# Optimization experiments

Hardware: AMD Instinct MI355X
Metric: run time of the kernel (lower is better)

## Reference

```python
import jax, jax.numpy as jnp
from jax import lax
import numpy as np

B, S, H = 8, 512, 768


def setup_inputs() -> dict:
    key = jax.random.key(0)
    ks = jax.random.split(key, 8)
    outputs = jax.random.normal(ks[0], (B, S, H), dtype=jnp.float32)
    starts = jax.random.randint(ks[1], (B,), S // 4, 3 * S // 4)
    mask = jnp.stack([starts, jnp.full((B,), S, dtype=starts.dtype)], axis=1)  # [B,2]
    sc = 1.0 / np.sqrt(H)
    Wa_w = jax.random.normal(ks[2], (H, H), dtype=jnp.float32) * sc
    Wa_b = jax.random.normal(ks[3], (H,), dtype=jnp.float32) * sc
    Ua_w = jax.random.normal(ks[4], (H, H), dtype=jnp.float32) * sc
    Ua_b = jax.random.normal(ks[5], (H,), dtype=jnp.float32) * sc
    Va_w = jax.random.normal(ks[6], (1, H), dtype=jnp.float32) * sc
    Va_b = jax.random.normal(ks[7], (1,), dtype=jnp.float32) * sc
    return {"outputs": outputs, "mask": mask, "Wa_w": Wa_w, "Wa_b": Wa_b,
            "Ua_w": Ua_w, "Ua_b": Ua_b, "Va_w": Va_w, "Va_b": Va_b}


def reference(outputs, mask, Wa_w, Wa_b, Ua_w, Ua_b, Va_w, Va_b):
    # outputs: [B,S,H]; mask[:,0] = start (source = tokens [0:start], summary = [start:S])
    b, s, h = outputs.shape
    Wq = jnp.einsum('bsh,oh->bso', outputs, Wa_w) + Wa_b  # query proj, [B,S,H]
    Uk = jnp.einsum('bsh,oh->bso', outputs, Ua_w) + Ua_b  # key proj,   [B,S,H]
    va = Va_w[0]  # [H]
    vb = Va_b[0]

    # Stream over query token positions to avoid a [B,S,S,H] tanh intermediate.
    def step(_, wq_t):  # wq_t: [B,H]
        m = jnp.tanh(wq_t[:, None, :] + Uk)          # [B,S,H]
        sc_t = jnp.einsum('bkh,h->bk', m, va) + vb   # [B,S]
        return None, sc_t

    _, scores = lax.scan(step, None, jnp.swapaxes(Wq, 0, 1))  # [S(query token), B, S(key)]
    scores = jnp.swapaxes(scores, 0, 1)  # [B, S_token, S_key]

    start = mask[:, 0]                              # [B]
    j = jnp.arange(s)
    # summary query j corresponds to token index start + j
    t_idx = jnp.clip(start[:, None] + j[None, :], 0, s - 1)            # [B,S]
    sc = jnp.take_along_axis(scores, t_idx[:, :, None], axis=1)       # [B,S,S]
    key_mask = (j[None, :] < start[:, None])                           # [B,S] valid source keys
    q_mask = (j[None, :] < (s - start)[:, None])                       # [B,S] valid summary queries

    sc = jnp.where(key_mask[:, None, :], sc, -1e30)
    w = jax.nn.softmax(sc, axis=-1)
    # zero out exactly where the torch code leaves zeros
    attentions = w * key_mask[:, None, :].astype(w.dtype) * q_mask[:, :, None].astype(w.dtype)
    contexts = jnp.einsum('bjk,bkh->bjh', attentions, outputs)
    return attentions, contexts
```

## Files before the change

kernel.cpp:

```cpp
#include <hip/hip_runtime.h>

typedef float  f32x4   __attribute__((ext_vector_type(4)));
typedef short  short8  __attribute__((ext_vector_type(8)));
typedef unsigned short ushort8 __attribute__((ext_vector_type(8)));

constexpr int kB = 8;
constexpr int kS = 512;
constexpr int kH = 768;

constexpr float kTanhScale = 2.8853900817779268f;

__device__ __forceinline__ float native_exp2(float x) {
    float r; asm("v_exp_f32 %0, %1" : "=v"(r) : "v"(x)); return r;
}

__device__ __forceinline__ float waveMax(float v) {
#pragma unroll
    for (int off = 32; off > 0; off >>= 1) v = fmaxf(v, __shfl_xor(v, off, 64));
    return v;
}
__device__ __forceinline__ float waveSum(float v) {
#pragma unroll
    for (int off = 32; off > 0; off >>= 1) v += __shfl_xor(v, off, 64);
    return v;
}

__device__ __forceinline__ void cvt16(const float4* v, unsigned short* hb, unsigned short* lb) {
#pragma unroll
    for (int q = 0; q < 4; ++q) {
#pragma unroll
        for (int c = 0; c < 4; ++c) {
            float x = (&v[q].x)[c];
            unsigned u = __float_as_uint(x);
            hb[q * 4 + c] = (unsigned short)(u >> 16);
            float hf = __uint_as_float(u & 0xFFFF0000u);
            lb[q * 4 + c] = (unsigned short)(__float_as_uint(x - hf) >> 16);
        }
    }
}

__global__ __launch_bounds__(256) void k1_mfma(
    const float* __restrict__ A,
    const float* __restrict__ W0, const float* __restrict__ b0,
    const float* __restrict__ W1, const float* __restrict__ b1,
    float* __restrict__ eq, float* __restrict__ ekT)
{
    __shared__ char smem[49664];
    unsigned short* Ahi = (unsigned short*)smem;
    unsigned short* Alo = (unsigned short*)(smem + 10240);
    unsigned short* Bhi = (unsigned short*)(smem + 20480);
    unsigned short* Blo = (unsigned short*)(smem + 28160);

    const int z = blockIdx.z;
    const float* W    = z ? W1 : W0;
    const float* bias = z ? b1 : b0;

    const int m0 = blockIdx.y * 128;
    const int n0 = blockIdx.x * 96;
    const int t  = threadIdx.x;

    const int ar = t >> 1, ko = (t & 1) << 4;
    const float* agp = A + (size_t)(m0 + ar) * kH + ko;
    const float* wgp = W + (size_t)(n0 + ar) * kH + ko;
    const bool doB = (ar < 96);

    const int wid = t >> 6, lane = t & 63;
    const int wr = wid >> 1, wc = wid & 1;
    const int lr = lane & 15, lk = (lane >> 4) << 3;

    f32x4 acc[4][3];
#pragma unroll
    for (int mi = 0; mi < 4; ++mi)
#pragma unroll
        for (int ni = 0; ni < 3; ++ni)
#pragma unroll
            for (int r = 0; r < 4; ++r) acc[mi][ni][r] = 0.0f;

    for (int h0 = 0; h0 < kH; h0 += 32) {
        float4 av[4], wv[4];
#pragma unroll
        for (int q = 0; q < 4; ++q) av[q] = *(const float4*)(agp + h0 + 4 * q);
        if (doB) {
#pragma unroll
            for (int q = 0; q < 4; ++q) wv[q] = *(const float4*)(wgp + h0 + 4 * q);
        }
        __syncthreads();
        {
            unsigned short hb[16], lb[16];
            cvt16(av, hb, lb);
            *(ushort8*)(Ahi + ar * 40 + ko)     = *(ushort8*)(hb);
            *(ushort8*)(Ahi + ar * 40 + ko + 8) = *(ushort8*)(hb + 8);
            *(ushort8*)(Alo + ar * 40 + ko)     = *(ushort8*)(lb);
            *(ushort8*)(Alo + ar * 40 + ko + 8) = *(ushort8*)(lb + 8);
            if (doB) {
                cvt16(wv, hb, lb);
                *(ushort8*)(Bhi + ar * 40 + ko)     = *(ushort8*)(hb);
                *(ushort8*)(Bhi + ar * 40 + ko + 8) = *(ushort8*)(hb + 8);
                *(ushort8*)(Blo + ar * 40 + ko)     = *(ushort8*)(lb);
                *(ushort8*)(Blo + ar * 40 + ko + 8) = *(ushort8*)(lb + 8);
            }
        }
        __syncthreads();

        short8 ah[4], al_[4], bh[3], bl[3];
#pragma unroll
        for (int mi = 0; mi < 4; ++mi) {
            const int row = wr * 64 + mi * 16 + lr;
            ah[mi]  = *(const short8*)(Ahi + row * 40 + lk);
            al_[mi] = *(const short8*)(Alo + row * 40 + lk);
        }
#pragma unroll
        for (int ni = 0; ni < 3; ++ni) {
            const int row = wc * 48 + ni * 16 + lr;
            bh[ni] = *(const short8*)(Bhi + row * 40 + lk);
            bl[ni] = *(const short8*)(Blo + row * 40 + lk);
        }
#pragma unroll
        for (int mi = 0; mi < 4; ++mi)
#pragma unroll
            for (int ni = 0; ni < 3; ++ni)
                acc[mi][ni] = __builtin_amdgcn_mfma_f32_16x16x32_bf16(ah[mi], bh[ni], acc[mi][ni], 0, 0, 0);
#pragma unroll
        for (int mi = 0; mi < 4; ++mi)
#pragma unroll
            for (int ni = 0; ni < 3; ++ni)
                acc[mi][ni] = __builtin_amdgcn_mfma_f32_16x16x32_bf16(al_[mi], bh[ni], acc[mi][ni], 0, 0, 0);
#pragma unroll
        for (int mi = 0; mi < 4; ++mi)
#pragma unroll
            for (int ni = 0; ni < 3; ++ni)
                acc[mi][ni] = __builtin_amdgcn_mfma_f32_16x16x32_bf16(ah[mi], bl[ni], acc[mi][ni], 0, 0, 0);
    }

    if (z == 0) {
#pragma unroll
        for (int mi = 0; mi < 4; ++mi)
#pragma unroll
            for (int ni = 0; ni < 3; ++ni) {
                const int mg = m0 + wr * 64 + mi * 16 + ((lane >> 4) << 2);
                const int ng = n0 + wc * 48 + ni * 16 + lr;
                const float bn = bias[ng];
#pragma unroll
                for (int r = 0; r < 4; ++r)
                    eq[(size_t)(mg + r) * kH + ng] = native_exp2((acc[mi][ni][r] + bn) * kTanhScale);
            }
    } else {
        __syncthreads();
        float* stg = (float*)smem;
#pragma unroll
        for (int mi = 0; mi < 4; ++mi)
#pragma unroll
            for (int ni = 0; ni < 3; ++ni) {
                const int ml = wr * 64 + mi * 16 + ((lane >> 4) << 2);
                const int nl = wc * 48 + ni * 16 + lr;
                const float bn = bias[n0 + nl];
#pragma unroll
                for (int r = 0; r < 4; ++r)
                    stg[(ml + r) * 97 + nl] = native_exp2((acc[mi][ni][r] + bn) * kTanhScale);
            }
        __syncthreads();
        const int bI = m0 >> 9, sb = m0 & (kS - 1);
        const int s4 = (t & 31) << 2, hb_ = t >> 5;
#pragma unroll
        for (int u = 0; u < 12; ++u) {
            const int h = (u << 3) + hb_;
            float4 o = { stg[(s4 + 0) * 97 + h], stg[(s4 + 1) * 97 + h],
                         stg[(s4 + 2) * 97 + h], stg[(s4 + 3) * 97 + h] };
            *(float4*)(ekT + ((size_t)bI * kH + n0 + h) * kS + sb + s4) = o;
        }
    }
}

__global__ void k2a_worklist(const int* __restrict__ mask, int* __restrict__ wl)
{
    __shared__ int ne[kB], off[kB];
    const int tid = threadIdx.x;
    if (tid < kB) {
        int start = mask[2 * tid];
        ne[tid] = ((kS - start + 1) >> 1) * ((start + 63) >> 6);
    }
    __syncthreads();
    if (tid == 0) {
        int s = 0;
        for (int b = 0; b < kB; ++b) { off[b] = s; s += ne[b]; }
        wl[0] = s;
    }
    __syncthreads();
    for (int b = 0; b < kB; ++b) {
        int start = mask[2 * b];
        int nkw = (start + 63) >> 6;
        int n = ne[b], base = off[b];
        for (int t = tid; t < n; t += blockDim.x) {
            int jt = t / nkw, kt = t - jt * nkw;
            wl[1 + base + t] = (b << 16) | (jt << 8) | kt;
        }
    }
}

__global__ __launch_bounds__(256) void k2_scores(
    const float* __restrict__ Eq, const float* __restrict__ EkT,
    const float* __restrict__ va, const int* __restrict__ mask,
    const int* __restrict__ wl, float* __restrict__ scores)
{
    const int ntiles = wl[0];
    const int lane = threadIdx.x & 63;
    const int wslot = (blockIdx.x << 2) | (threadIdx.x >> 6);
    const int nslots = gridDim.x << 2;

    for (int w = wslot; w < ntiles; w += nslots) {
        const int e = __builtin_amdgcn_readfirstlane(wl[1 + w]);
        const int b = e >> 16, jt = (e >> 8) & 255, kt = e & 255;
        const int start = __builtin_amdgcn_readfirstlane(mask[2 * b]);
        const int jmax = kS - start;
        const int j0 = jt << 1, k0 = kt << 6;

        const float* ekp = EkT + (size_t)b * kH * kS + k0 + lane;
        int t0 = start + j0;     if (t0 > kS - 1) t0 = kS - 1;
        int t1 = start + j0 + 1; if (t1 > kS - 1) t1 = kS - 1;
        const float* eq0 = Eq + ((size_t)b * kS + t0) * kH;
        const float* eq1 = Eq + ((size_t)b * kS + t1) * kH;

        float a0 = 0.0f, a1 = 0.0f;
        float eA[8], eB[8];
#pragma unroll
        for (int c = 0; c < 8; ++c) eA[c] = ekp[(size_t)c * kS];
#pragma unroll
        for (int c = 0; c < 8; ++c) eB[c] = ekp[(size_t)(8 + c) * kS];

        for (int h0 = 0; h0 < kH; h0 += 16) {
            const bool more = (h0 + 16) < kH;
            float nA[8], nB[8];
            if (more) {
#pragma unroll
                for (int c = 0; c < 8; ++c) nA[c] = ekp[(size_t)(h0 + 16 + c) * kS];
            }
#pragma unroll
            for (int c = 0; c < 8; ++c) {
                const float vc = va[h0 + c];
                float r0 = __builtin_amdgcn_rcpf(fmaf(eq0[h0 + c], eA[c], 1.0f));
                float r1 = __builtin_amdgcn_rcpf(fmaf(eq1[h0 + c], eA[c], 1.0f));
                a0 = fmaf(vc, r0, a0);
                a1 = fmaf(vc, r1, a1);
            }
            if (more) {
#pragma unroll
                for (int c = 0; c < 8; ++c) nB[c] = ekp[(size_t)(h0 + 24 + c) * kS];
#pragma unroll
                for (int c = 0; c < 8; ++c) {
                    const float vc = va[h0 + 8 + c];
                    float r0 = __builtin_amdgcn_rcpf(fmaf(eq0[h0 + 8 + c], eB[c], 1.0f));
                    float r1 = __builtin_amdgcn_rcpf(fmaf(eq1[h0 + 8 + c], eB[c], 1.0f));
                    a0 = fmaf(vc, r0, a0);
                    a1 = fmaf(vc, r1, a1);
                }
#pragma unroll
                for (int c = 0; c < 8; ++c) { eA[c] = nA[c]; eB[c] = nB[c]; }
            } else {
#pragma unroll
                for (int c = 0; c < 8; ++c) {
                    const float vc = va[h0 + 8 + c];
                    float r0 = __builtin_amdgcn_rcpf(fmaf(eq0[h0 + 8 + c], eB[c], 1.0f));
                    float r1 = __builtin_amdgcn_rcpf(fmaf(eq1[h0 + 8 + c], eB[c], 1.0f));
                    a0 = fmaf(vc, r0, a0);
                    a1 = fmaf(vc, r1, a1);
                }
            }
        }

        float* srow = scores + ((size_t)b * kS + j0) * kS + k0 + lane;
        if (j0 < jmax)     srow[0]  = -2.0f * a0;
        if (j0 + 1 < jmax) srow[kS] = -2.0f * a1;
    }
}

__global__ __launch_bounds__(256) void k3_softmax(
    float* __restrict__ attn, const int* __restrict__ mask)
{
    const int bx = blockIdx.x;
    const int b = bx >> 9;
    const int j = bx & (kS - 1);
    const int start = mask[2 * b];
    float* row = attn + ((size_t)b * kS + j) * kS;
    const int tid = threadIdx.x;

    if (j >= kS - start) {
        row[tid] = 0.0f;
        row[tid + 256] = 0.0f;
        return;
    }

    float v0 = (tid < start) ? row[tid] : -1e30f;
    float v1 = (tid + 256 < start) ? row[tid + 256] : -1e30f;

    __shared__ float red[4];
    const int wid = tid >> 6;

    float m = waveMax(fmaxf(v0, v1));
    if ((tid & 63) == 0) red[wid] = m;
    __syncthreads();
    m = fmaxf(fmaxf(red[0], red[1]), fmaxf(red[2], red[3]));
    __syncthreads();

    float e0 = (tid < start) ? __expf(v0 - m) : 0.0f;
    float e1 = (tid + 256 < start) ? __expf(v1 - m) : 0.0f;
    float s = waveSum(e0 + e1);
    if ((tid & 63) == 0) red[wid] = s;
    __syncthreads();
    s = red[0] + red[1] + red[2] + red[3];

    float inv = __builtin_amdgcn_rcpf(s);
    row[tid] = e0 * inv;
    row[tid + 256] = e1 * inv;
}

__global__ __launch_bounds__(256) void k4_context(
    const float* __restrict__ attn, const float* __restrict__ outs,
    const int* __restrict__ mask, float* __restrict__ ctx)
{
    const int b = blockIdx.z;
    const int start = mask[2 * b];
    const int kmax = (start + 15) & ~15;
    const int m0 = blockIdx.y * 64;
    const int n0 = blockIdx.x * 64;

    __shared__ float As[16][68];
    __shared__ float Bs[16][68];

    const int tid = threadIdx.x;
    const int lrow = tid >> 2;
    const int lk4  = (tid & 3) << 2;
    const int brow = tid >> 4;
    const int bh4  = (tid & 15) << 2;
    const int is = tid >> 4;
    const int js = tid & 15;

    const float* arow = attn + ((size_t)b * kS + m0 + lrow) * kS + lk4;
    const float* bbase = outs + (size_t)b * kS * kH + n0 + bh4;

    float acc[4][4] = {};

    for (int k0 = 0; k0 < kmax; k0 += 16) {
        float4 av = *(const float4*)(arow + k0);
        float4 bv = *(const float4*)(bbase + (size_t)(k0 + brow) * kH);
        __syncthreads();
        As[lk4 + 0][lrow] = av.x;
        As[lk4 + 1][lrow] = av.y;
        As[lk4 + 2][lrow] = av.z;
        As[lk4 + 3][lrow] = av.w;
        *(float4*)&Bs[brow][bh4] = bv;
        __syncthreads();
#pragma unroll
        for (int kk = 0; kk < 16; ++kk) {
            const float* ap = &As[kk][is << 2];
            const float* bp = &Bs[kk][js << 2];
            float aa[4], bb[4];
#pragma unroll
            for (int c = 0; c < 4; ++c) { aa[c] = ap[c]; bb[c] = bp[c]; }
#pragma unroll
            for (int i = 0; i < 4; ++i)
#pragma unroll
                for (int j = 0; j < 4; ++j)
                    acc[i][j] = fmaf(aa[i], bb[j], acc[i][j]);
        }
    }

#pragma unroll
    for (int i = 0; i < 4; ++i) {
        int row = m0 + (is << 2) + i;
        float4 o = {acc[i][0], acc[i][1], acc[i][2], acc[i][3]};
        *(float4*)(ctx + ((size_t)b * kS + row) * kH + n0 + (js << 2)) = o;
    }
}

extern "C" void kernel_launch(void* const* d_in, const int* in_sizes, int n_in,
                              void* d_out, int out_size, void* d_ws, size_t ws_size,
                              hipStream_t stream)
{
    const float* outputs = (const float*)d_in[0];
    const int*   mask    = (const int*)d_in[1];
    const float* Wa_w    = (const float*)d_in[2];
    const float* Wa_b    = (const float*)d_in[3];
    const float* Ua_w    = (const float*)d_in[4];
    const float* Ua_b    = (const float*)d_in[5];
    const float* Va_w    = (const float*)d_in[6];

    float* attn = (float*)d_out;
    float* ctx  = attn + (size_t)kB * kS * kS;
    float* EkT  = ctx;

    constexpr size_t kWlBytes = 64 * 1024;
    int* wl = (int*)d_ws;
    float* Eq = (float*)((char*)d_ws + kWlBytes);

    k1_mfma<<<dim3(kH / 96, (kB * kS) / 128, 2), 256, 0, stream>>>(
        outputs, Wa_w, Wa_b, Ua_w, Ua_b, Eq, EkT);

    k2a_worklist<<<dim3(1), 256, 0, stream>>>(mask, wl);
    k2_scores<<<dim3(1024), 256, 0, stream>>>(Eq, EkT, Va_w, mask, wl, attn);

    k3_softmax<<<dim3(kB * kS), 256, 0, stream>>>(attn, mask);

    k4_context<<<dim3(kH / 64, kS / 64, kB), 256, 0, stream>>>(attn, outputs, mask, ctx);
}
```

Baseline: 161.0 us.

## Pre-split inputs to bf16 hi/lo, skip unneeded projection tiles, split scores over H

A new pre-pass kernel converts the activations and both weight matrices once into bf16 hi/lo pairs, so the GEMM no longer repeats that split per tile. The projection GEMM now exits early for row tiles that only cover masked query or key positions, and it writes compacted Eq/EkT buffers indexed by summary and source position. The score kernel splits the hidden dimension into two halves, which doubles the number of work items, writes two partial score buffers, and has the softmax add them. The cost is an extra launch, extra traffic for the converted copies and partial buffers, and scratch space borrowed from the output buffers.

```diff
diff --git a/kernel.cpp b/kernel.cpp
--- a/kernel.cpp
+++ b/kernel.cpp
@@ -7,6 +7,7 @@
 constexpr int kB = 8;
 constexpr int kS = 512;
 constexpr int kH = 768;
+constexpr int kJM = 384;
 
 constexpr float kTanhScale = 2.8853900817779268f;
 
@@ -25,25 +26,39 @@
     return v;
 }
 
-__device__ __forceinline__ void cvt16(const float4* v, unsigned short* hb, unsigned short* lb) {
-#pragma unroll
-    for (int q = 0; q < 4; ++q) {
-#pragma unroll
-        for (int c = 0; c < 4; ++c) {
-            float x = (&v[q].x)[c];
-            unsigned u = __float_as_uint(x);
-            hb[q * 4 + c] = (unsigned short)(u >> 16);
-            float hf = __uint_as_float(u & 0xFFFF0000u);
-            lb[q * 4 + c] = (unsigned short)(__float_as_uint(x - hf) >> 16);
-        }
-    }
+__global__ __launch_bounds__(256) void k0_convert(
+    const float* __restrict__ X, const float* __restrict__ Wa, const float* __restrict__ Ua,
+    unsigned short* __restrict__ Xhi, unsigned short* __restrict__ Xlo,
+    unsigned short* __restrict__ Wahi, unsigned short* __restrict__ Walo,
+    unsigned short* __restrict__ Uahi, unsigned short* __restrict__ Ualo)
+{
+    const int i4 = blockIdx.x * 256 + threadIdx.x;
+    const float* src; unsigned short *hi, *lo; int off;
+    if (i4 < 786432)      { src = X;  hi = Xhi;  lo = Xlo;  off = i4; }
+    else if (i4 < 933888) { src = Wa; hi = Wahi; lo = Walo; off = i4 - 786432; }
+    else                  { src = Ua; hi = Uahi; lo = Ualo; off = i4 - 933888; }
+
+    float4 v = *(const float4*)(src + (size_t)off * 4);
+    unsigned short h[4], l[4];
+#pragma unroll
+    for (int c = 0; c < 4; ++c) {
+        float x = (&v.x)[c];
+        unsigned u = __float_as_uint(x);
+        h[c] = (unsigned short)(u >> 16);
+        float hf = __uint_as_float(u & 0xFFFF0000u);
+        l[c] = (unsigned short)(__float_as_uint(x - hf) >> 16);
+    }
+    *(ushort4*)(hi + (size_t)off * 4) = make_ushort4(h[0], h[1], h[2], h[3]);
+    *(ushort4*)(lo + (size_t)off * 4) = make_ushort4(l[0], l[1], l[2], l[3]);
 }
 
 __global__ __launch_bounds__(256) void k1_mfma(
-    const float* __restrict__ A,
-    const float* __restrict__ W0, const float* __restrict__ b0,
-    const float* __restrict__ W1, const float* __restrict__ b1,
-    float* __restrict__ eq, float* __restrict__ ekT)
+    const unsigned short* __restrict__ Xhi, const unsigned short* __restrict__ Xlo,
+    const unsigned short* __restrict__ W0hi, const unsigned short* __restrict__ W0lo,
+    const unsigned short* __restrict__ W1hi, const unsigned short* __restrict__ W1lo,
+    const float* __restrict__ b0, const float* __restrict__ b1,
+    const int* __restrict__ mask,
+    float* __restrict__ Eqc, float* __restrict__ EkTc)
 {
     __shared__ char smem[49664];
     unsigned short* Ahi = (unsigned short*)smem;
@@ -52,17 +67,24 @@
     unsigned short* Blo = (unsigned short*)(smem + 28160);
 
     const int z = blockIdx.z;
-    const float* W    = z ? W1 : W0;
+    const unsigned short* Whi = z ? W1hi : W0hi;
+    const unsigned short* Wlo = z ? W1lo : W0lo;
     const float* bias = z ? b1 : b0;
 
     const int m0 = blockIdx.y * 128;
     const int n0 = blockIdx.x * 96;
     const int t  = threadIdx.x;
+    const int bI = m0 >> 9;
+    const int lb = m0 & (kS - 1);
+    const int start = mask[2 * bI];
+
+    if (z == 0) { if (lb + 128 <= start) return; }
+    else        { if (lb >= start) return; }
 
     const int ar = t >> 1, ko = (t & 1) << 4;
-    const float* agp = A + (size_t)(m0 + ar) * kH + ko;
-    const float* wgp = W + (size_t)(n0 + ar) * kH + ko;
     const bool doB = (ar < 96);
+    const size_t aoff = (size_t)(m0 + ar) * kH + ko;
+    const size_t woff = (size_t)(n0 + ar) * kH + ko;
 
     const int wid = t >> 6, lane = t & 63;
     const int wr = wid >> 1, wc = wid & 1;
@@ -77,28 +99,27 @@
             for (int r = 0; r < 4; ++r) acc[mi][ni][r] = 0.0f;
 
     for (int h0 = 0; h0 < kH; h0 += 32) {
-        float4 av[4], wv[4];
-#pragma unroll
-        for (int q = 0; q < 4; ++q) av[q] = *(const float4*)(agp + h0 + 4 * q);
+        ushort8 ah0 = *(const ushort8*)(Xhi + aoff + h0);
+        ushort8 ah1 = *(const ushort8*)(Xhi + aoff + h0 + 8);
+        ushort8 al0 = *(const ushort8*)(Xlo + aoff + h0);
+        ushort8 al1 = *(const ushort8*)(Xlo + aoff + h0 + 8);
+        ushort8 bh0, bh1, bl0, bl1;
         if (doB) {
-#pragma unroll
-            for (int q = 0; q < 4; ++q) wv[q] = *(const float4*)(wgp + h0 + 4 * q);
-        }
-        __syncthreads();
-        {
-            unsigned short hb[16], lb[16];
-            cvt16(av, hb, lb);
-            *(ushort8*)(Ahi + ar * 40 + ko)     = *(ushort8*)(hb);
-            *(ushort8*)(Ahi + ar * 40 + ko + 8) = *(ushort8*)(hb + 8);
-            *(ushort8*)(Alo + ar * 40 + ko)     = *(ushort8*)(lb);
-            *(ushort8*)(Alo + ar * 40 + ko + 8) = *(ushort8*)(lb + 8);
-            if (doB) {
-                cvt16(wv, hb, lb);
-                *(ushort8*)(Bhi + ar * 40 + ko)     = *(ushort8*)(hb);
-                *(ushort8*)(Bhi + ar * 40 + ko + 8) = *(ushort8*)(hb + 8);
-                *(ushort8*)(Blo + ar * 40 + ko)     = *(ushort8*)(lb);
-                *(ushort8*)(Blo + ar * 40 + ko + 8) = *(ushort8*)(lb + 8);
-            }
+            bh0 = *(const ushort8*)(Whi + woff + h0);
+            bh1 = *(const ushort8*)(Whi + woff + h0 + 8);
+            bl0 = *(const ushort8*)(Wlo + woff + h0);
+            bl1 = *(const ushort8*)(Wlo + woff + h0 + 8);
+        }
+        __syncthreads();
+        *(ushort8*)(Ahi + ar * 40 + ko)     = ah0;
+        *(ushort8*)(Ahi + ar * 40 + ko + 8) = ah1;
+        *(ushort8*)(Alo + ar * 40 + ko)     = al0;
+        *(ushort8*)(Alo + ar * 40 + ko + 8) = al1;
+        if (doB) {
+            *(ushort8*)(Bhi + ar * 40 + ko)     = bh0;
+            *(ushort8*)(Bhi + ar * 40 + ko + 8) = bh1;
+            *(ushort8*)(Blo + ar * 40 + ko)     = bl0;
+            *(ushort8*)(Blo + ar * 40 + ko + 8) = bl1;
         }
         __syncthreads();
 
@@ -137,12 +158,16 @@
         for (int mi = 0; mi < 4; ++mi)
 #pragma unroll
             for (int ni = 0; ni < 3; ++ni) {
-                const int mg = m0 + wr * 64 + mi * 16 + ((lane >> 4) << 2);
+                const int ml = lb + wr * 64 + mi * 16 + ((lane >> 4) << 2);
                 const int ng = n0 + wc * 48 + ni * 16 + lr;
                 const float bn = bias[ng];
 #pragma unroll
-                for (int r = 0; r < 4; ++r)
-                    eq[(size_t)(mg + r) * kH + ng] = native_exp2((acc[mi][ni][r] + bn) * kTanhScale);
+                for (int r = 0; r < 4; ++r) {
+                    const int jj = ml + r - start;
+                    if (jj >= 0)
+                        Eqc[((size_t)bI * kJM + jj) * kH + ng] =
+                            native_exp2((acc[mi][ni][r] + bn) * kTanhScale);
+                }
             }
     } else {
         __syncthreads();
@@ -159,14 +184,21 @@
                     stg[(ml + r) * 97 + nl] = native_exp2((acc[mi][ni][r] + bn) * kTanhScale);
             }
         __syncthreads();
-        const int bI = m0 >> 9, sb = m0 & (kS - 1);
         const int s4 = (t & 31) << 2, hb_ = t >> 5;
+        const int sg = lb + s4;
 #pragma unroll
         for (int u = 0; u < 12; ++u) {
             const int h = (u << 3) + hb_;
-            float4 o = { stg[(s4 + 0) * 97 + h], stg[(s4 + 1) * 97 + h],
-                         stg[(s4 + 2) * 97 + h], stg[(s4 + 3) * 97 + h] };
-            *(float4*)(ekT + ((size_t)bI * kH + n0 + h) * kS + sb + s4) = o;
+            float o[4] = { stg[(s4 + 0) * 97 + h], stg[(s4 + 1) * 97 + h],
+                           stg[(s4 + 2) * 97 + h], stg[(s4 + 3) * 97 + h] };
+            float* dst = EkTc + ((size_t)bI * kH + n0 + h) * kJM + sg;
+            if (sg + 3 < start) {
+                *(float4*)dst = make_float4(o[0], o[1], o[2], o[3]);
+            } else {
+#pragma unroll
+                for (int e2 = 0; e2 < 4; ++e2)
+                    if (sg + e2 < start) dst[e2] = o[e2];
+            }
         }
     }
 }
@@ -177,7 +209,7 @@
     const int tid = threadIdx.x;
     if (tid < kB) {
         int start = mask[2 * tid];
-        ne[tid] = ((kS - start + 1) >> 1) * ((start + 63) >> 6);
+        ne[tid] = ((kS - start + 1) >> 1) * ((start + 63) >> 6) * 2;
     }
     __syncthreads();
     if (tid == 0) {
@@ -191,16 +223,17 @@
         int nkw = (start + 63) >> 6;
         int n = ne[b], base = off[b];
         for (int t = tid; t < n; t += blockDim.x) {
-            int jt = t / nkw, kt = t - jt * nkw;
-            wl[1 + base + t] = (b << 16) | (jt << 8) | kt;
+            int c = t & 1, p = t >> 1;
+            int jt = p / nkw, kt = p - jt * nkw;
+            wl[1 + base + t] = (b << 16) | (jt << 8) | (kt << 1) | c;
         }
     }
 }
 
 __global__ __launch_bounds__(256) void k2_scores(
-    const float* __restrict__ Eq, const float* __restrict__ EkT,
+    const float* __restrict__ Eqc, const float* __restrict__ EkTc,
     const float* __restrict__ va, const int* __restrict__ mask,
-    const int* __restrict__ wl, float* __restrict__ scores)
+    const int* __restrict__ wl, float* __restrict__ part0, float* __restrict__ part1)
 {
     const int ntiles = wl[0];
     const int lane = threadIdx.x & 63;
@@ -209,72 +242,74 @@
 
     for (int w = wslot; w < ntiles; w += nslots) {
         const int e = __builtin_amdgcn_readfirstlane(wl[1 + w]);
-        const int b = e >> 16, jt = (e >> 8) & 255, kt = e & 255;
+        const int b = e >> 16, jt = (e >> 8) & 255, ktc = e & 255;
+        const int kt = ktc >> 1, c = ktc & 1;
         const int start = __builtin_amdgcn_readfirstlane(mask[2 * b]);
         const int jmax = kS - start;
         const int j0 = jt << 1, k0 = kt << 6;
-
-        const float* ekp = EkT + (size_t)b * kH * kS + k0 + lane;
-        int t0 = start + j0;     if (t0 > kS - 1) t0 = kS - 1;
-        int t1 = start + j0 + 1; if (t1 > kS - 1) t1 = kS - 1;
-        const float* eq0 = Eq + ((size_t)b * kS + t0) * kH;
-        const float* eq1 = Eq + ((size_t)b * kS + t1) * kH;
+        const int hbase = c * 384;
+
+        const float* eq0 = Eqc + ((size_t)b * kJM + j0) * kH + hbase;
+        const float* eq1 = eq0 + kH;
+        const float* ekp = EkTc + ((size_t)b * kH + hbase) * kJM + k0 + lane;
+        const float* vap = va + hbase;
 
         float a0 = 0.0f, a1 = 0.0f;
         float eA[8], eB[8];
 #pragma unroll
-        for (int c = 0; c < 8; ++c) eA[c] = ekp[(size_t)c * kS];
-#pragma unroll
-        for (int c = 0; c < 8; ++c) eB[c] = ekp[(size_t)(8 + c) * kS];
-
-        for (int h0 = 0; h0 < kH; h0 += 16) {
-            const bool more = (h0 + 16) < kH;
+        for (int c2 = 0; c2 < 8; ++c2) eA[c2] = ekp[(size_t)c2 * kJM];
+#pragma unroll
+        for (int c2 = 0; c2 < 8; ++c2) eB[c2] = ekp[(size_t)(8 + c2) * kJM];
+
+        for (int h0 = 0; h0 < 384; h0 += 16) {
+            const bool more = (h0 + 16) < 384;
             float nA[8], nB[8];
             if (more) {
 #pragma unroll
-                for (int c = 0; c < 8; ++c) nA[c] = ekp[(size_t)(h0 + 16 + c) * kS];
-            }
-#pragma unroll
-            for (int c = 0; c < 8; ++c) {
-                const float vc = va[h0 + c];
-                float r0 = __builtin_amdgcn_rcpf(fmaf(eq0[h0 + c], eA[c], 1.0f));
-                float r1 = __builtin_amdgcn_rcpf(fmaf(eq1[h0 + c], eA[c], 1.0f));
+                for (int c2 = 0; c2 < 8; ++c2) nA[c2] = ekp[(size_t)(h0 + 16 + c2) * kJM];
+            }
+#pragma unroll
+            for (int c2 = 0; c2 < 8; ++c2) {
+                const float vc = vap[h0 + c2];
+                float r0 = __builtin_amdgcn_rcpf(fmaf(eq0[h0 + c2], eA[c2], 1.0f));
+                float r1 = __builtin_amdgcn_rcpf(fmaf(eq1[h0 + c2], eA[c2], 1.0f));
                 a0 = fmaf(vc, r0, a0);
                 a1 = fmaf(vc, r1, a1);
             }
             if (more) {
 #pragma unroll
-                for (int c = 0; c < 8; ++c) nB[c] = ekp[(size_t)(h0 + 24 + c) * kS];
-#pragma unroll
-                for (int c = 0; c < 8; ++c) {
-                    const float vc = va[h0 + 8 + c];
-                    float r0 = __builtin_amdgcn_rcpf(fmaf(eq0[h0 + 8 + c], eB[c], 1.0f));
-                    float r1 = __builtin_amdgcn_rcpf(fmaf(eq1[h0 + 8 + c], eB[c], 1.0f));
+                for (int c2 = 0; c2 < 8; ++c2) nB[c2] = ekp[(size_t)(h0 + 24 + c2) * kJM];
+#pragma unroll
+                for (int c2 = 0; c2 < 8; ++c2) {
+                    const float vc = vap[h0 + 8 + c2];
+                    float r0 = __builtin_amdgcn_rcpf(fmaf(eq0[h0 + 8 + c2], eB[c2], 1.0f));
+                    float r1 = __builtin_amdgcn_rcpf(fmaf(eq1[h0 + 8 + c2], eB[c2], 1.0f));
                     a0 = fmaf(vc, r0, a0);
                     a1 = fmaf(vc, r1, a1);
                 }
 #pragma unroll
-                for (int c = 0; c < 8; ++c) { eA[c] = nA[c]; eB[c] = nB[c]; }
+                for (int c2 = 0; c2 < 8; ++c2) { eA[c2] = nA[c2]; eB[c2] = nB[c2]; }
             } else {
 #pragma unroll
-                for (int c = 0; c < 8; ++c) {
-                    const float vc = va[h0 + 8 + c];
-                    float r0 = __builtin_amdgcn_rcpf(fmaf(eq0[h0 + 8 + c], eB[c], 1.0f));
-                    float r1 = __builtin_amdgcn_rcpf(fmaf(eq1[h0 + 8 + c], eB[c], 1.0f));
+                for (int c2 = 0; c2 < 8; ++c2) {
+                    const float vc = vap[h0 + 8 + c2];
+                    float r0 = __builtin_amdgcn_rcpf(fmaf(eq0[h0 + 8 + c2], eB[c2], 1.0f));
+                    float r1 = __builtin_amdgcn_rcpf(fmaf(eq1[h0 + 8 + c2], eB[c2], 1.0f));
                     a0 = fmaf(vc, r0, a0);
                     a1 = fmaf(vc, r1, a1);
                 }
             }
         }
 
-        float* srow = scores + ((size_t)b * kS + j0) * kS + k0 + lane;
+        float* srow = (c ? part1 : part0) + ((size_t)b * kS + j0) * kS + k0 + lane;
         if (j0 < jmax)     srow[0]  = -2.0f * a0;
         if (j0 + 1 < jmax) srow[kS] = -2.0f * a1;
     }
 }
 
 __global__ __launch_bounds__(256) void k3_softmax(
-    float* __restrict__ attn, const int* __restrict__ mask)
+    float* __restrict__ attn, const float* __restrict__ part1,
+    const int* __restrict__ mask)
 {
     const int bx = blockIdx.x;
     const int b = bx >> 9;
@@ -289,8 +324,9 @@
         return;
     }
 
-    float v0 = (tid < start) ? row[tid] : -1e30f;
-    float v1 = (tid + 256 < start) ? row[tid + 256] : -1e30f;
+    const float* p1row = part1 + ((size_t)b * kS + j) * kS;
+    float v0 = (tid < start) ? row[tid] + p1row[tid] : -1e30f;
+    float v1 = (tid + 256 < start) ? row[tid + 256] + p1row[tid + 256] : -1e30f;
 
     __shared__ float red[4];
     const int wid = tid >> 6;
@@ -386,19 +422,29 @@
 
     float* attn = (float*)d_out;
     float* ctx  = attn + (size_t)kB * kS * kS;
-    float* EkT  = ctx;
-
-    constexpr size_t kWlBytes = 64 * 1024;
+
+    unsigned short* Xhi  = (unsigned short*)ctx;
+    unsigned short* Xlo  = Xhi + (size_t)kB * kS * kH;
+    unsigned short* Wahi = (unsigned short*)attn;
+    unsigned short* Walo = Wahi + (size_t)kH * kH;
+    unsigned short* Uahi = Walo + (size_t)kH * kH;
+    unsigned short* Ualo = Uahi + (size_t)kH * kH;
+    float* part1 = ctx;
+
     int* wl = (int*)d_ws;
-    float* Eq = (float*)((char*)d_ws + kWlBytes);
+    float* Eqc  = (float*)((char*)d_ws + 131072);
+    float* EkTc = Eqc + (size_t)kB * kJM * kH;
+
+    k0_convert<<<dim3(4224), 256, 0, stream>>>(
+        outputs, Wa_w, Ua_w, Xhi, Xlo, Wahi, Walo, Uahi, Ualo);
 
     k1_mfma<<<dim3(kH / 96, (kB * kS) / 128, 2), 256, 0, stream>>>(
-        outputs, Wa_w, Wa_b, Ua_w, Ua_b, Eq, EkT);
+        Xhi, Xlo, Wahi, Walo, Uahi, Ualo, Wa_b, Ua_b, mask, Eqc, EkTc);
 
     k2a_worklist<<<dim3(1), 256, 0, stream>>>(mask, wl);
-    k2_scores<<<dim3(1024), 256, 0, stream>>>(Eq, EkT, Va_w, mask, wl, attn);
-
-    k3_softmax<<<dim3(kB * kS), 256, 0, stream>>>(attn, mask);
+    k2_scores<<<dim3(2048), 256, 0, stream>>>(Eqc, EkTc, Va_w, mask, wl, attn, part1);
+
+    k3_softmax<<<dim3(kB * kS), 256, 0, stream>>>(attn, part1, mask);
 
     k4_context<<<dim3(kH / 64, kS / 64, kB), 256, 0, stream>>>(attn, outputs, mask, ctx);
 }
```

New measurement: 152.0 us. 1.06x faster.
